# Kernel optimization log

Measured on AMD Instinct MI355X. Metric: run time of the kernel, lower is better.

The kernel has to match this reference:

```python
import jax, jax.numpy as jnp
import numpy as np
from jax import lax

KEEP_RATIO = 0.5
GROUP_RATIO = 0.5
TOPK = 2


def setup_inputs() -> dict:
    key = jax.random.key(0)
    k1, k2, k3 = jax.random.split(key, 3)
    x = jax.random.normal(k1, (64, 577, 768), dtype=jnp.float32)
    cls_attn = jax.random.uniform(k2, (64, 576), dtype=jnp.float32)
    expert_distribution = jax.random.uniform(k3, (64, 577, 16), dtype=jnp.float32)
    return {"x": x, "cls_attn": cls_attn, "expert_distribution": expert_distribution}


def _build_graph(spa, B, S, k):
    """Cosine kNN graph per batch + to_undirected dedup + iterative directional
    degree filter (KthAverageAggregator.directional_filter). Returns fixed-size
    candidate edge arrays (src, dst) with a validity mask."""
    Nn = B * S
    # cosine similarity kNN (pyg knn_graph cosine=True, loop=False)
    cn = spa / jnp.clip(jnp.linalg.norm(spa, axis=-1, keepdims=True), 1e-12)
    sim = jnp.einsum('bse,bte->bst', cn, cn)                    # [B,S,S]
    sim = jnp.where(jnp.eye(S, dtype=bool)[None], -2.0, sim)    # exclude self
    _, nbr = lax.top_k(sim, k)                                  # [B,S,k] neighbors j of node i
    offs = (jnp.arange(B) * S)[:, None, None]
    src = (nbr + offs).reshape(-1)                              # flow source_to_target: edge (j -> i)
    dst = jnp.broadcast_to(jnp.arange(S)[None, :, None] + offs, (B, S, k)).reshape(-1)
    # to_undirected with coalesce (dedup) -> fixed-size candidates + unique mask
    cs = jnp.concatenate([src, dst])
    cd = jnp.concatenate([dst, src])
    keyv = cs * Nn + cd
    perm = jnp.argsort(keyv)
    es, ed, ks = cs[perm], cd[perm], keyv[perm]
    uniq = jnp.concatenate([jnp.array([True]), ks[1:] != ks[:-1]])

    def deg_in(m):
        return jax.ops.segment_sum(m.astype(jnp.int32), ed, num_segments=Nn)

    # directional filter: keep edge (u->v) iff in_degree[v] > in_degree[u]; iterate to fixpoint
    d0 = deg_in(uniq)
    cur0 = uniq & (d0[ed] > d0[es])

    def cond(st):
        return st[0].sum() != st[1]

    def body(st):
        cur, _ = st
        d = deg_in(cur)
        return (cur & (d[ed] > d[es]), cur.sum())

    valid, _ = lax.while_loop(cond, body, (cur0, jnp.int32(-1)))
    return es, ed, valid


def reference(x, cls_attn, expert_distribution):
    B, Np1, D = x.shape
    N = Np1 - 1
    cls_tk = x[:, :1]                     # [B,1,D]
    patch_x = x[:, 1:]                    # [B,N,D]
    ped = expert_distribution[:, 1:]      # [B,N,E]
    # cls_attn_reordering: sort patches by cls attention, descending
    order = jnp.argsort(-cls_attn, axis=1)
    ca = jnp.take_along_axis(cls_attn, order, axis=1)
    px = jnp.take_along_axis(patch_x, order[:, :, None], axis=1)
    ped = jnp.take_along_axis(ped, order[:, :, None], axis=1)
    density = int(N * KEEP_RATIO)
    S = N - density
    patch_tk, skip = px[:, :density], px[:, density:]
    nsca, sca = ca[:, :density], ca[:, density:]
    spa = ped[:, density:]                # skip tokens' expert distributions (kNN criteria)
    Nn = B * S

    es, ed, valid = _build_graph(spa, B, S, TOPK)

    # propagate (sum aggregation) with self loops
    xs = skip.reshape(Nn, D)
    w = valid.astype(xs.dtype)[:, None]
    avg = jax.ops.segment_sum(xs[es] * w, ed, num_segments=Nn) + xs
    avg = avg.reshape(B, S, D)

    # node degree over edges[0] (sources), self loops add 1
    deg_src = jax.ops.segment_sum(valid.astype(jnp.int32), es, num_segments=Nn) + 1
    nd = deg_src.reshape(B, S)
    G = int(S * GROUP_RATIO)
    _, gidx = lax.top_k(nd, G)            # [B,G]

    summ = jnp.take_along_axis(avg, gidx[:, :, None], axis=1)
    sca_sel = jnp.take_along_axis(sca, gidx, axis=1)
    tokens = jnp.concatenate([cls_tk, patch_tk, summ], axis=1)
    attn = jnp.concatenate([nsca, sca_sel], axis=-1)
    return tokens, attn
```

## Files before the change

### kernel.cpp

```cpp
#include <hip/hip_runtime.h>
#include <hip/hip_bf16.h>
#include <math.h>

#define BB   64
#define NP1  577
#define DD   768
#define NNP  576
#define DENS 288
#define SS   288
#define KNN  2
#define EPB  (SS*KNN*2)
#define GG   144
#define TOK  (1+DENS+GG)
#define ATT  (DENS+GG)
#define TPB  576

__global__ __launch_bounds__(TPB) void k_graph(const float* __restrict__ ca,
                                               const float* __restrict__ ex,
                                               int* __restrict__ order_g,
                                               unsigned* __restrict__ rowptr,
                                               unsigned* __restrict__ col,
                                               int* __restrict__ selnode,
                                               int* __restrict__ selrow,
                                               float* __restrict__ out_attn) {
    __shared__ float    val[NNP];
    __shared__ float    sortedv[NNP];
    __shared__ short    sorder[NNP];
    __shared__ float    cn[SS][17];
    __shared__ short    nbrs[SS][2];
    __shared__ unsigned edge[EPB];
    __shared__ unsigned char act[EPB];
    __shared__ unsigned deg[SS];
    __shared__ unsigned indeg[SS];
    __shared__ int      ndv[SS];
    __shared__ unsigned scan[NNP];
    __shared__ int      srow[SS];
    __shared__ short    gsel[GG];
    __shared__ int      changed;
    const int b = blockIdx.x, t = threadIdx.x;

    float v = ca[b*NNP + t];
    val[t] = v;
    __syncthreads();
    int rank = 0;
    #pragma unroll 8
    for (int m = 0; m < NNP; m++) {
        float u = val[m];
        rank += (u > v) || (u == v && m < t);
    }
    sortedv[rank] = v;
    sorder[rank]  = (short)t;
    if (rank < DENS) order_g[b*NNP + rank] = t;
    __syncthreads();

    if (t < DENS) out_attn[b*ATT + t] = sortedv[t];

    if (t < SS) {
        int src = sorder[DENS + t];
        int row = b*NP1 + 1 + src;
        srow[t] = row;
        const float* rp = ex + (size_t)row * 16;
        float vv[16]; float ssum = 0.f;
        #pragma unroll
        for (int e = 0; e < 16; e++) { vv[e] = rp[e]; ssum += vv[e]*vv[e]; }
        float inv = 1.0f / fmaxf(sqrtf(ssum), 1e-12f);
        #pragma unroll
        for (int e = 0; e < 16; e++) cn[t][e] = vv[e]*inv;
    }
    __syncthreads();

    if (t < SS) {
        float my[16];
        #pragma unroll
        for (int e = 0; e < 16; e++) my[e] = cn[t][e];
        float v1 = -3.f, v2 = -3.f; int i1 = -1, i2 = -1;
        for (int j = 0; j < SS; j++) {
            if (j == t) continue;
            float s = 0.f;
            #pragma unroll
            for (int e = 0; e < 16; e++) s = fmaf(my[e], cn[j][e], s);
            if (s > v1)      { v2 = v1; i2 = i1; v1 = s; i1 = j; }
            else if (s > v2) { v2 = s;  i2 = j; }
        }
        nbrs[t][0] = (short)i1; nbrs[t][1] = (short)i2;
    }
    __syncthreads();

    if (t < SS) {
        #pragma unroll
        for (int j = 0; j < 2; j++) {
            int p = nbrs[t][j];
            bool mutual = (nbrs[p][0] == t) || (nbrs[p][1] == t);
            unsigned char pv = (!mutual || (t < p)) ? 1 : 0;
            int q = (t*2 + j) * 2;
            edge[q]   = ((unsigned)p << 16) | (unsigned)t;
            edge[q+1] = ((unsigned)t << 16) | (unsigned)p;
            act[q] = pv; act[q+1] = pv;
        }
    }
    __syncthreads();

    while (true) {
        if (t < SS) deg[t] = 0;
        if (t == 0) changed = 0;
        __syncthreads();
        #pragma unroll
        for (int e = t; e < EPB; e += TPB)
            if (act[e]) atomicAdd(&deg[edge[e] & 0xFFFFu], 1u);
        __syncthreads();
        #pragma unroll
        for (int e = t; e < EPB; e += TPB) {
            if (act[e]) {
                unsigned ed = edge[e];
                if (!(deg[ed & 0xFFFFu] > deg[ed >> 16])) { act[e] = 0; changed = 1; }
            }
        }
        __syncthreads();
        int ch = changed;
        __syncthreads();
        if (!ch) break;
    }
    if (t < SS) indeg[t] = deg[t];
    __syncthreads();

    if (t < SS) deg[t] = 0;
    __syncthreads();
    #pragma unroll
    for (int e = t; e < EPB; e += TPB)
        if (act[e]) atomicAdd(&deg[edge[e] >> 16], 1u);
    __syncthreads();
    if (t < SS) ndv[t] = (int)deg[t] + 1;
    __syncthreads();

    if (t < SS) {
        int mine = ndv[t], r = 0;
        for (int m = 0; m < SS; m++) {
            int u = ndv[m];
            r += (u > mine) || (u == mine && m < t);
        }
        if (r < GG) gsel[r] = (short)t;
    }
    __syncthreads();

    if (t < GG) {
        int n = gsel[t];
        selnode[b*GG + t] = n;
        selrow[b*GG + t]  = srow[n];
        out_attn[b*ATT + DENS + t] = sortedv[DENS + n];
    }

    unsigned dv = (t < SS) ? indeg[t] : 0u;
    scan[t] = dv;
    __syncthreads();
    for (int off = 1; off < SS; off <<= 1) {
        unsigned add = (t >= off) ? scan[t - off] : 0u;
        __syncthreads();
        scan[t] += add;
        __syncthreads();
    }
    if (t < SS) {
        rowptr[b*(SS+1) + t + 1] = scan[t];
        deg[t] = scan[t] - dv;
    }
    if (t == 0) rowptr[b*(SS+1)] = 0;
    __syncthreads();

    #pragma unroll
    for (int e = t; e < EPB; e += TPB) {
        if (act[e]) {
            unsigned ed = edge[e];
            unsigned pos = atomicAdd(&deg[ed & 0xFFFFu], 1u);
            col[b*EPB + pos] = (unsigned)srow[ed >> 16];
        }
    }
}

__global__ __launch_bounds__(256) void k_tokens(const float* __restrict__ x,
                                                const int* __restrict__ order,
                                                const int* __restrict__ selnode,
                                                const int* __restrict__ selrow,
                                                const unsigned* __restrict__ rowptr,
                                                const unsigned* __restrict__ col,
                                                float* __restrict__ out) {
    const int wid  = threadIdx.x >> 6;
    const int lane = threadIdx.x & 63;
    int row = blockIdx.x*4 + wid;
    if (row >= BB*TOK) return;
    int b  = row / TOK;
    int tk = row - b*TOK;
    float4* __restrict__ orow = (float4*)(out + (size_t)row*DD);

    if (tk <= DENS) {
        int srcrow = (tk == 0) ? (b*NP1) : (b*NP1 + 1 + order[b*NNP + (tk-1)]);
        const float4* s4 = (const float4*)(x + (size_t)srcrow*DD);
        #pragma unroll
        for (int q = 0; q < 3; q++) orow[lane + q*64] = s4[lane + q*64];
    } else {
        int r = tk - 1 - DENS;
        int n = selnode[b*GG + r];
        int g = b*(SS+1) + n;
        unsigned e0 = rowptr[g], e1 = rowptr[g+1];
        float4 acc0 = make_float4(0,0,0,0), acc1 = acc0, acc2 = acc0;
        for (unsigned e = e0; e < e1; e++) {
            const float4* s4 = (const float4*)(x + (size_t)col[b*EPB + e]*DD);
            float4 a = s4[lane], bq = s4[lane + 64], c = s4[lane + 128];
            acc0.x += a.x;  acc0.y += a.y;  acc0.z += a.z;  acc0.w += a.w;
            acc1.x += bq.x; acc1.y += bq.y; acc1.z += bq.z; acc1.w += bq.w;
            acc2.x += c.x;  acc2.y += c.y;  acc2.z += c.z;  acc2.w += c.w;
        }
        const float4* s4 = (const float4*)(x + (size_t)selrow[b*GG + r]*DD);
        float4 a = s4[lane], bq = s4[lane + 64], c = s4[lane + 128];
        acc0.x += a.x;  acc0.y += a.y;  acc0.z += a.z;  acc0.w += a.w;
        acc1.x += bq.x; acc1.y += bq.y; acc1.z += bq.z; acc1.w += bq.w;
        acc2.x += c.x;  acc2.y += c.y;  acc2.z += c.z;  acc2.w += c.w;
        orow[lane]       = acc0;
        orow[lane + 64]  = acc1;
        orow[lane + 128] = acc2;
    }
}

extern "C" void kernel_launch(void* const* d_in, const int* in_sizes, int n_in,
                              void* d_out, int out_size, void* d_ws, size_t ws_size,
                              hipStream_t stream) {
    const float* x  = (const float*)d_in[0];
    const float* ca = (const float*)d_in[1];
    const float* ex = (const float*)d_in[2];
    float* out = (float*)d_out;

    char* w = (char*)d_ws;
    int*      order   = (int*)w;      w += (size_t)BB*NNP*4;
    unsigned* rowptr  = (unsigned*)w; w += (size_t)BB*(SS+1)*4;
    unsigned* col     = (unsigned*)w; w += (size_t)BB*EPB*4;
    int*      selnode = (int*)w;      w += (size_t)BB*GG*4;
    int*      selrow  = (int*)w;      w += (size_t)BB*GG*4;

    float* out_attn = out + (size_t)BB*TOK*DD;

    k_graph<<<BB, TPB, 0, stream>>>(ca, ex, order, rowptr, col,
                                    selnode, selrow, out_attn);
    k_tokens<<<(BB*TOK + 3)/4, 256, 0, stream>>>(x, order, selnode, selrow,
                                                 rowptr, col, out);
}
```

Measured before the change: 282.2 us.

## Split kNN and degree-rank loops across both thread halves, vectorize shared reads

The kNN similarity scan and the group top-k ranking now use all 576 threads, where before only 288 did any work. Each half of the block scans half the candidates, and the partial top-2 results and partial ranks are merged through shared memory. Shared-memory reads are vectorized to float4/int4, and the fixpoint loop uses __syncthreads_count instead of a shared flag with two barriers. The change adds extra shared buffers and a merge barrier, and the merge must reproduce the original tie-breaking exactly.

Result: faster. 247.6 us (-12.2%).

```diff
diff --git a/kernel.cpp b/kernel.cpp
--- a/kernel.cpp
+++ b/kernel.cpp
@@ -14,6 +14,7 @@
 #define TOK  (1+DENS+GG)
 #define ATT  (DENS+GG)
 #define TPB  576
+#define HALF 144
 
 __global__ __launch_bounds__(TPB) void k_graph(const float* __restrict__ ca,
                                                const float* __restrict__ ex,
@@ -23,34 +24,45 @@
                                                int* __restrict__ selnode,
                                                int* __restrict__ selrow,
                                                float* __restrict__ out_attn) {
-    __shared__ float    val[NNP];
+    __shared__ __align__(16) float val[NNP];
     __shared__ float    sortedv[NNP];
     __shared__ short    sorder[NNP];
-    __shared__ float    cn[SS][17];
+    __shared__ float4   cn4[SS][4];
     __shared__ short    nbrs[SS][2];
     __shared__ unsigned edge[EPB];
     __shared__ unsigned char act[EPB];
     __shared__ unsigned deg[SS];
     __shared__ unsigned indeg[SS];
-    __shared__ int      ndv[SS];
+    __shared__ __align__(16) int ndv[SS];
     __shared__ unsigned scan[NNP];
     __shared__ int      srow[SS];
     __shared__ short    gsel[GG];
-    __shared__ int      changed;
+    __shared__ float    cval[2][SS][2];
+    __shared__ short    cidx[2][SS][2];
+    __shared__ short    rankp[2][SS];
     const int b = blockIdx.x, t = threadIdx.x;
+    const int h  = (t >= SS) ? 1 : 0;
+    const int n  = t - h*SS;
 
     float v = ca[b*NNP + t];
     val[t] = v;
     __syncthreads();
-    int rank = 0;
-    #pragma unroll 8
-    for (int m = 0; m < NNP; m++) {
-        float u = val[m];
-        rank += (u > v) || (u == v && m < t);
-    }
-    sortedv[rank] = v;
-    sorder[rank]  = (short)t;
-    if (rank < DENS) order_g[b*NNP + rank] = t;
+    {
+        const float4* v4 = (const float4*)val;
+        int rank = 0;
+        #pragma unroll 4
+        for (int m4 = 0; m4 < NNP/4; m4++) {
+            float4 u = v4[m4];
+            int m = m4*4;
+            rank += (u.x > v) || (u.x == v && m   < t);
+            rank += (u.y > v) || (u.y == v && m+1 < t);
+            rank += (u.z > v) || (u.z == v && m+2 < t);
+            rank += (u.w > v) || (u.w == v && m+3 < t);
+        }
+        sortedv[rank] = v;
+        sorder[rank]  = (short)t;
+        if (rank < DENS) order_g[b*NNP + rank] = t;
+    }
     __syncthreads();
 
     if (t < DENS) out_attn[b*ATT + t] = sortedv[t];
@@ -59,30 +71,59 @@
         int src = sorder[DENS + t];
         int row = b*NP1 + 1 + src;
         srow[t] = row;
-        const float* rp = ex + (size_t)row * 16;
-        float vv[16]; float ssum = 0.f;
-        #pragma unroll
-        for (int e = 0; e < 16; e++) { vv[e] = rp[e]; ssum += vv[e]*vv[e]; }
+        const float4* rp = (const float4*)(ex + (size_t)row * 16);
+        float4 f0 = rp[0], f1 = rp[1], f2 = rp[2], f3 = rp[3];
+        float ssum = f0.x*f0.x + f0.y*f0.y + f0.z*f0.z + f0.w*f0.w
+                   + f1.x*f1.x + f1.y*f1.y + f1.z*f1.z + f1.w*f1.w
+                   + f2.x*f2.x + f2.y*f2.y + f2.z*f2.z + f2.w*f2.w
+                   + f3.x*f3.x + f3.y*f3.y + f3.z*f3.z + f3.w*f3.w;
         float inv = 1.0f / fmaxf(sqrtf(ssum), 1e-12f);
-        #pragma unroll
-        for (int e = 0; e < 16; e++) cn[t][e] = vv[e]*inv;
-    }
-    __syncthreads();
-
-    if (t < SS) {
-        float my[16];
-        #pragma unroll
-        for (int e = 0; e < 16; e++) my[e] = cn[t][e];
+        f0.x*=inv; f0.y*=inv; f0.z*=inv; f0.w*=inv;
+        f1.x*=inv; f1.y*=inv; f1.z*=inv; f1.w*=inv;
+        f2.x*=inv; f2.y*=inv; f2.z*=inv; f2.w*=inv;
+        f3.x*=inv; f3.y*=inv; f3.z*=inv; f3.w*=inv;
+        cn4[t][0]=f0; cn4[t][1]=f1; cn4[t][2]=f2; cn4[t][3]=f3;
+    }
+    __syncthreads();
+
+    {
+        const float4 m0 = cn4[n][0], m1 = cn4[n][1], m2 = cn4[n][2], m3 = cn4[n][3];
         float v1 = -3.f, v2 = -3.f; int i1 = -1, i2 = -1;
-        for (int j = 0; j < SS; j++) {
-            if (j == t) continue;
-            float s = 0.f;
+        const int jbeg = h*HALF;
+        #pragma unroll 2
+        for (int j = jbeg; j < jbeg + HALF; j += 4) {
+            float sq[4];
             #pragma unroll
-            for (int e = 0; e < 16; e++) s = fmaf(my[e], cn[j][e], s);
-            if (s > v1)      { v2 = v1; i2 = i1; v1 = s; i1 = j; }
-            else if (s > v2) { v2 = s;  i2 = j; }
-        }
-        nbrs[t][0] = (short)i1; nbrs[t][1] = (short)i2;
+            for (int q = 0; q < 4; q++) {
+                const float4 a0 = cn4[j+q][0], a1 = cn4[j+q][1],
+                             a2 = cn4[j+q][2], a3 = cn4[j+q][3];
+                float s = m0.x*a0.x;
+                s = fmaf(m0.y,a0.y,s); s = fmaf(m0.z,a0.z,s); s = fmaf(m0.w,a0.w,s);
+                s = fmaf(m1.x,a1.x,s); s = fmaf(m1.y,a1.y,s); s = fmaf(m1.z,a1.z,s); s = fmaf(m1.w,a1.w,s);
+                s = fmaf(m2.x,a2.x,s); s = fmaf(m2.y,a2.y,s); s = fmaf(m2.z,a2.z,s); s = fmaf(m2.w,a2.w,s);
+                s = fmaf(m3.x,a3.x,s); s = fmaf(m3.y,a3.y,s); s = fmaf(m3.z,a3.z,s); s = fmaf(m3.w,a3.w,s);
+                sq[q] = (j+q == n) ? -3.f : s;
+            }
+            #pragma unroll
+            for (int q = 0; q < 4; q++) {
+                if (sq[q] > v1)      { v2 = v1; i2 = i1; v1 = sq[q]; i1 = j+q; }
+                else if (sq[q] > v2) { v2 = sq[q]; i2 = j+q; }
+            }
+        }
+        cval[h][n][0] = v1; cval[h][n][1] = v2;
+        cidx[h][n][0] = (short)i1; cidx[h][n][1] = (short)i2;
+    }
+    __syncthreads();
+
+    if (t < SS) {
+        float a1 = cval[0][t][0], a2 = cval[0][t][1];
+        float b1 = cval[1][t][0], b2 = cval[1][t][1];
+        short ia1 = cidx[0][t][0], ia2 = cidx[0][t][1];
+        short ib1 = cidx[1][t][0], ib2 = cidx[1][t][1];
+        short j1, j2;
+        if (b1 > a1) { j1 = ib1; j2 = (b2 > a1) ? ib2 : ia1; }
+        else         { j1 = ia1; j2 = (b1 > a2) ? ib1 : ia2; }
+        nbrs[t][0] = j1; nbrs[t][1] = j2;
     }
     __syncthreads();
 
@@ -100,25 +141,22 @@
     }
     __syncthreads();
 
-    while (true) {
+    for (;;) {
         if (t < SS) deg[t] = 0;
-        if (t == 0) changed = 0;
         __syncthreads();
         #pragma unroll
         for (int e = t; e < EPB; e += TPB)
             if (act[e]) atomicAdd(&deg[edge[e] & 0xFFFFu], 1u);
         __syncthreads();
+        int removed = 0;
         #pragma unroll
         for (int e = t; e < EPB; e += TPB) {
             if (act[e]) {
                 unsigned ed = edge[e];
-                if (!(deg[ed & 0xFFFFu] > deg[ed >> 16])) { act[e] = 0; changed = 1; }
+                if (!(deg[ed & 0xFFFFu] > deg[ed >> 16])) { act[e] = 0; removed = 1; }
             }
         }
-        __syncthreads();
-        int ch = changed;
-        __syncthreads();
-        if (!ch) break;
+        if (__syncthreads_count(removed) == 0) break;
     }
     if (t < SS) indeg[t] = deg[t];
     __syncthreads();
@@ -132,21 +170,34 @@
     if (t < SS) ndv[t] = (int)deg[t] + 1;
     __syncthreads();
 
-    if (t < SS) {
-        int mine = ndv[t], r = 0;
-        for (int m = 0; m < SS; m++) {
-            int u = ndv[m];
-            r += (u > mine) || (u == mine && m < t);
-        }
+    {
+        const int4* nd4 = (const int4*)ndv;
+        int mine = ndv[n];
+        int r = 0;
+        const int m4beg = h*(HALF/4);
+        #pragma unroll 4
+        for (int m4 = m4beg; m4 < m4beg + HALF/4; m4++) {
+            int4 u = nd4[m4];
+            int m = m4*4;
+            r += (u.x > mine) || (u.x == mine && m   < n);
+            r += (u.y > mine) || (u.y == mine && m+1 < n);
+            r += (u.z > mine) || (u.z == mine && m+2 < n);
+            r += (u.w > mine) || (u.w == mine && m+3 < n);
+        }
+        rankp[h][n] = (short)r;
+    }
+    __syncthreads();
+    if (t < SS) {
+        int r = (int)rankp[0][t] + (int)rankp[1][t];
         if (r < GG) gsel[r] = (short)t;
     }
     __syncthreads();
 
     if (t < GG) {
-        int n = gsel[t];
-        selnode[b*GG + t] = n;
-        selrow[b*GG + t]  = srow[n];
-        out_attn[b*ATT + DENS + t] = sortedv[DENS + n];
+        int nn = gsel[t];
+        selnode[b*GG + t] = nn;
+        selrow[b*GG + t]  = srow[nn];
+        out_attn[b*ATT + DENS + t] = sortedv[DENS + nn];
     }
 
     unsigned dv = (t < SS) ? indeg[t] : 0u;
```
